# Kernel optimization log

Measured on AMD Instinct MI355X. Metric: run time of the kernel, lower is better.

The kernel has to match this reference:

```python
import jax, jax.numpy as jnp
import numpy as np

# Module config (from init_kwargs)
KH, KW = 3, 3          # kernel_size
SH, SW = 2, 2          # stride
PH, PW = 1, 1          # padding
EPS = 1e-8             # temperature clamp eps
DEN_EPS = 1e-12        # denominator stabilizer (hardcoded in kornia)
DN = ('NCHW', 'OIHW', 'NCHW')


def _window_grid_kernel(kh, kw):
    # window coordinates residual to window center, normalized to [-1, 1]
    ys, xs = jnp.meshgrid(jnp.arange(kh, dtype=jnp.float32),
                          jnp.arange(kw, dtype=jnp.float32), indexing='ij')
    gx = xs * (2.0 / (kw - 1)) - 1.0
    gy = ys * (2.0 / (kh - 1)) - 1.0
    return jnp.stack([gx, gy], axis=0)[:, None]  # (2,1,kh,kw), ch0=x, ch1=y


def _center_kernel(kh, kw):
    k = jnp.zeros((2, 2, kh, kw), jnp.float32)
    k = k.at[0, 0, kh // 2, kw // 2].set(1.0)
    k = k.at[1, 1, kh // 2, kw // 2].set(1.0)
    return k  # (2,2,kh,kw)


def _sum_pool(x):
    # pool_coef * avg_pool2d(count_include_pad=True) == windowed sum with zero pad
    return jax.lax.reduce_window(x, 0.0, jax.lax.add,
                                 (1, 1, KH, KW), (1, 1, SH, SW),
                                 [(0, 0), (0, 0), (PH, PH), (PW, PW)])


def setup_inputs() -> dict:
    key = jax.random.key(0)
    x = jax.random.normal(key, (8, 16, 512, 512), dtype=jnp.float32)
    temperature = jnp.ones((), dtype=jnp.float32)
    return {"x": x, "temperature": temperature}


def reference(x, temperature):
    b, c, h, w = x.shape
    xf = x.reshape(b * c, 1, h, w)

    x_exp = jnp.exp(xf / jnp.maximum(temperature, EPS))

    den = _sum_pool(x_exp) + DEN_EPS                     # (BC,1,Ho,Wo)
    resp_maxima = _sum_pool(x_exp * xf) / den            # softmax-pooled values

    # weighted sum of window-relative coordinates
    coords_num = jax.lax.conv_general_dilated(
        x_exp, _window_grid_kernel(KH, KW), (SH, SW),
        [(PH, PH), (PW, PW)], dimension_numbers=DN)      # (BC,2,Ho,Wo)

    # global grid (x, y) pixel coordinates, center-picked per window
    ys, xs = jnp.meshgrid(jnp.arange(h, dtype=jnp.float32),
                          jnp.arange(w, dtype=jnp.float32), indexing='ij')
    grid_global = jnp.stack([xs, ys], axis=0)[None]      # (1,2,h,w)
    grid_pooled = jax.lax.conv_general_dilated(
        grid_global, _center_kernel(KH, KW), (SH, SW),
        [(PH, PH), (PW, PW)], dimension_numbers=DN)      # (1,2,Ho,Wo)

    coords_max = coords_num / den + grid_pooled          # broadcast over BC

    # normalized_coordinates=True: map pixel coords to [-1, 1]
    cx = coords_max[:, 0] * (2.0 / (w - 1)) - 1.0
    cy = coords_max[:, 1] * (2.0 / (h - 1)) - 1.0
    coords_max = jnp.stack([cx, cy], axis=1)             # (BC,2,Ho,Wo)

    return coords_max, resp_maxima
```

## Files before the change

### kernel.cpp

```cpp
#include <hip/hip_runtime.h>


#define H  512
#define W  512
#define HO 256
#define WO 256
#define BC 128

typedef float v2f __attribute__((ext_vector_type(2)));

__global__ __launch_bounds__(256) void casm_kernel(
    const float* __restrict__ x, const float* __restrict__ temp,
    float* __restrict__ out)
{
    int nblk = gridDim.x;
    int bid  = blockIdx.x;
    int swz  = (bid & 7) * (nblk >> 3) + (bid >> 3);

    int idx = swz * 256 + (int)threadIdx.x;
    int t   = idx & 127;
    int ho  = (idx >> 7) & (HO - 1);
    int bc  = idx >> 15;

    float k = 1.44269504088896340736f / fmaxf(temp[0], 1e-8f);

    const float* __restrict__ xp = x + (size_t)bc * (H * W);
    int r0 = 2 * ho - 1;
    int cM = 4 * t;
    float mL = (t == 0) ? 0.0f : 1.0f;

    float den_a = 0.f, den_b = 0.f, cyn_a = 0.f, cyn_b = 0.f;
    float colL_a = 0.f, colR_a = 0.f, colL_b = 0.f, colR_b = 0.f;
    float num_a = 0.f, num_b = 0.f;

#pragma unroll
    for (int rr = 0; rr < 3; ++rr) {
        if (rr == 0 && r0 < 0) continue;
        const float* __restrict__ row = xp + (r0 + rr) * W;
        float4 v = *(const float4*)(row + cM);
        float vL = __shfl_up(v.w, 1);
        if ((t & 63) == 0 && t != 0) vL = row[cM - 1];
        float eL = mL * __builtin_amdgcn_exp2f(k * vL);
        float e0 = __builtin_amdgcn_exp2f(k * v.x);
        float e1 = __builtin_amdgcn_exp2f(k * v.y);
        float e2 = __builtin_amdgcn_exp2f(k * v.z);
        float e3 = __builtin_amdgcn_exp2f(k * v.w);
        float rs_a = eL + e0 + e1;
        float rs_b = e1 + e2 + e3;
        den_a += rs_a;  den_b += rs_b;
        if (rr == 0) { cyn_a -= rs_a; cyn_b -= rs_b; }
        if (rr == 2) { cyn_a += rs_a; cyn_b += rs_b; }
        colL_a += eL;  colR_a += e1;
        colL_b += e1;  colR_b += e3;
        num_a = fmaf(eL, vL, fmaf(e0, v.x, fmaf(e1, v.y, num_a)));
        num_b = fmaf(e1, v.y, fmaf(e2, v.z, fmaf(e3, v.w, num_b)));
    }

    float ia = __builtin_amdgcn_rcpf(den_a + 1e-12f);
    float ib = __builtin_amdgcn_rcpf(den_b + 1e-12f);
    const float scale = 2.0f / 511.0f;
    int wo0 = 2 * t;
    v2f vx = { ((colR_a - colL_a) * ia + (float)(2 * wo0    )) * scale - 1.0f,
               ((colR_b - colL_b) * ib + (float)(2 * wo0 + 2)) * scale - 1.0f };
    v2f vy = { (cyn_a * ia + (float)(2 * ho)) * scale - 1.0f,
               (cyn_b * ib + (float)(2 * ho)) * scale - 1.0f };
    v2f vr = { num_a * ia, num_b * ib };

    size_t pix   = (size_t)ho * WO + wo0;
    size_t cbase = (size_t)bc * (2 * HO * WO) + pix;
    __builtin_nontemporal_store(vx, (v2f*)(out + cbase));
    __builtin_nontemporal_store(vy, (v2f*)(out + cbase + HO * WO));
    __builtin_nontemporal_store(vr, (v2f*)(out + (size_t)BC * 2 * HO * WO
                                           + (size_t)bc * HO * WO + pix));
}

extern "C" void kernel_launch(void* const* d_in, const int* in_sizes, int n_in,
                              void* d_out, int out_size, void* d_ws, size_t ws_size,
                              hipStream_t stream) {
    const float* x    = (const float*)d_in[0];
    const float* temp = (const float*)d_in[1];
    float* out        = (float*)d_out;

    int total  = BC * HO * (WO / 2);
    int blocks = total / 256;
    casm_kernel<<<blocks, 256, 0, stream>>>(x, temp, out);
}
```

Baseline: 222.2 us.

## Compute two output rows per thread to share overlapping input row

Each thread now handles two vertically adjacent output rows, loading five input rows instead of three per output row, so the shared middle row's loads and exp computations are reused. The left-neighbour exp and product are shuffled from the adjacent lane instead of recomputing the exp, and nontemporal stores are replaced by plain float2 stores. This cuts redundant global reads and transcendental work by about a sixth and halves the grid, at the cost of more registers per thread and fewer threads in flight.

```diff
diff --git a/kernel.cpp b/kernel.cpp
--- a/kernel.cpp
+++ b/kernel.cpp
@@ -6,8 +6,6 @@
 #define HO 256
 #define WO 256
 #define BC 128
-
-typedef float v2f __attribute__((ext_vector_type(2)));
 
 __global__ __launch_bounds__(256) void casm_kernel(
     const float* __restrict__ x, const float* __restrict__ temp,
@@ -19,59 +17,101 @@
 
     int idx = swz * 256 + (int)threadIdx.x;
     int t   = idx & 127;
-    int ho  = (idx >> 7) & (HO - 1);
-    int bc  = idx >> 15;
+    int hp  = (idx >> 7) & 127;
+    int bc  = idx >> 14;
 
     float k = 1.44269504088896340736f / fmaxf(temp[0], 1e-8f);
 
     const float* __restrict__ xp = x + (size_t)bc * (H * W);
-    int r0 = 2 * ho - 1;
-    int cM = 4 * t;
-    float mL = (t == 0) ? 0.0f : 1.0f;
+    int  cM   = 4 * t;
+    float mL  = (t == 0) ? 0.0f : 1.0f;
+    bool bfix = ((t & 63) == 0) && (t != 0);
+    bool r0ok = (hp != 0);
 
-    float den_a = 0.f, den_b = 0.f, cyn_a = 0.f, cyn_b = 0.f;
-    float colL_a = 0.f, colR_a = 0.f, colL_b = 0.f, colR_b = 0.f;
-    float num_a = 0.f, num_b = 0.f;
+    const float* __restrict__ rb = xp + (size_t)(4 * hp) * W + cM;
+    float4 v0 = make_float4(0.f, 0.f, 0.f, 0.f);
+    if (r0ok) v0 = *(const float4*)(rb - W);
+    float4 v1 = *(const float4*)(rb);
+    float4 v2 = *(const float4*)(rb + W);
+    float4 v3 = *(const float4*)(rb + 2 * W);
+    float4 v4 = *(const float4*)(rb + 3 * W);
 
-#pragma unroll
-    for (int rr = 0; rr < 3; ++rr) {
-        if (rr == 0 && r0 < 0) continue;
-        const float* __restrict__ row = xp + (r0 + rr) * W;
-        float4 v = *(const float4*)(row + cM);
-        float vL = __shfl_up(v.w, 1);
-        if ((t & 63) == 0 && t != 0) vL = row[cM - 1];
-        float eL = mL * __builtin_amdgcn_exp2f(k * vL);
-        float e0 = __builtin_amdgcn_exp2f(k * v.x);
-        float e1 = __builtin_amdgcn_exp2f(k * v.y);
-        float e2 = __builtin_amdgcn_exp2f(k * v.z);
-        float e3 = __builtin_amdgcn_exp2f(k * v.w);
-        float rs_a = eL + e0 + e1;
-        float rs_b = e1 + e2 + e3;
-        den_a += rs_a;  den_b += rs_b;
-        if (rr == 0) { cyn_a -= rs_a; cyn_b -= rs_b; }
-        if (rr == 2) { cyn_a += rs_a; cyn_b += rs_b; }
-        colL_a += eL;  colR_a += e1;
-        colL_b += e1;  colR_b += e3;
-        num_a = fmaf(eL, vL, fmaf(e0, v.x, fmaf(e1, v.y, num_a)));
-        num_b = fmaf(e1, v.y, fmaf(e2, v.z, fmaf(e3, v.w, num_b)));
+#define EXPK(u) __builtin_amdgcn_exp2f(k * (u))
+#define ROW(v, rowp, rsA, rsB, dxA, dxB, nA, nB) {                       \
+        float e0 = EXPK((v).x), e1 = EXPK((v).y);                        \
+        float e2 = EXPK((v).z), e3 = EXPK((v).w);                        \
+        float p3 = e3 * (v).w;                                           \
+        float eL = __shfl_up(e3, 1);                                     \
+        float pL = __shfl_up(p3, 1);                                     \
+        if (bfix) { float vl = (rowp)[-1]; eL = EXPK(vl); pL = eL * vl; } \
+        eL *= mL; pL *= mL;                                              \
+        rsA = eL + e0 + e1;  rsB = e1 + e2 + e3;                         \
+        dxA = e1 - eL;       dxB = e3 - e1;                              \
+        nA  = pL + fmaf(e0, (v).x, e1 * (v).y);                          \
+        nB  = fmaf(e1, (v).y, fmaf(e2, (v).z, p3)); }
+
+    float rsA, rsB, dxA, dxB, nA, nB;
+
+    float d0A = 0, d0B = 0, cy0A = 0, cy0B = 0, x0A = 0, x0B = 0, m0A = 0, m0B = 0;
+    float d1A = 0, d1B = 0, cy1A = 0, cy1B = 0, x1A = 0, x1B = 0, m1A = 0, m1B = 0;
+
+    if (r0ok) {
+        ROW(v0, rb - W, rsA, rsB, dxA, dxB, nA, nB);
+        d0A += rsA; d0B += rsB; cy0A -= rsA; cy0B -= rsB;
+        x0A += dxA; x0B += dxB; m0A += nA;  m0B += nB;
     }
+    {
+        ROW(v1, rb, rsA, rsB, dxA, dxB, nA, nB);
+        d0A += rsA; d0B += rsB; x0A += dxA; x0B += dxB; m0A += nA; m0B += nB;
+    }
+    {
+        ROW(v2, rb + W, rsA, rsB, dxA, dxB, nA, nB);
+        d0A += rsA; d0B += rsB; cy0A += rsA; cy0B += rsB;
+        x0A += dxA; x0B += dxB; m0A += nA;  m0B += nB;
+        d1A += rsA; d1B += rsB; cy1A -= rsA; cy1B -= rsB;
+        x1A += dxA; x1B += dxB; m1A += nA;  m1B += nB;
+    }
+    {
+        ROW(v3, rb + 2 * W, rsA, rsB, dxA, dxB, nA, nB);
+        d1A += rsA; d1B += rsB; x1A += dxA; x1B += dxB; m1A += nA; m1B += nB;
+    }
+    {
+        ROW(v4, rb + 3 * W, rsA, rsB, dxA, dxB, nA, nB);
+        d1A += rsA; d1B += rsB; cy1A += rsA; cy1B += rsB;
+        x1A += dxA; x1B += dxB; m1A += nA;  m1B += nB;
+    }
+#undef ROW
+#undef EXPK
 
-    float ia = __builtin_amdgcn_rcpf(den_a + 1e-12f);
-    float ib = __builtin_amdgcn_rcpf(den_b + 1e-12f);
     const float scale = 2.0f / 511.0f;
     int wo0 = 2 * t;
-    v2f vx = { ((colR_a - colL_a) * ia + (float)(2 * wo0    )) * scale - 1.0f,
-               ((colR_b - colL_b) * ib + (float)(2 * wo0 + 2)) * scale - 1.0f };
-    v2f vy = { (cyn_a * ia + (float)(2 * ho)) * scale - 1.0f,
-               (cyn_b * ib + (float)(2 * ho)) * scale - 1.0f };
-    v2f vr = { num_a * ia, num_b * ib };
+    int ho0 = 2 * hp;
 
-    size_t pix   = (size_t)ho * WO + wo0;
-    size_t cbase = (size_t)bc * (2 * HO * WO) + pix;
-    __builtin_nontemporal_store(vx, (v2f*)(out + cbase));
-    __builtin_nontemporal_store(vy, (v2f*)(out + cbase + HO * WO));
-    __builtin_nontemporal_store(vr, (v2f*)(out + (size_t)BC * 2 * HO * WO
-                                           + (size_t)bc * HO * WO + pix));
+    float i0A = __builtin_amdgcn_rcpf(d0A + 1e-12f);
+    float i0B = __builtin_amdgcn_rcpf(d0B + 1e-12f);
+    float i1A = __builtin_amdgcn_rcpf(d1A + 1e-12f);
+    float i1B = __builtin_amdgcn_rcpf(d1B + 1e-12f);
+
+    size_t pix0  = (size_t)ho0 * WO + wo0;
+    size_t cbase = (size_t)bc * (2 * HO * WO);
+    size_t rbase = (size_t)BC * 2 * HO * WO + (size_t)bc * HO * WO;
+
+    *(float2*)(out + cbase + pix0) =
+        make_float2((x0A * i0A + (float)(2 * wo0)) * scale - 1.0f,
+                    (x0B * i0B + (float)(2 * wo0 + 2)) * scale - 1.0f);
+    *(float2*)(out + cbase + HO * WO + pix0) =
+        make_float2((cy0A * i0A + (float)(2 * ho0)) * scale - 1.0f,
+                    (cy0B * i0B + (float)(2 * ho0)) * scale - 1.0f);
+    *(float2*)(out + rbase + pix0) = make_float2(m0A * i0A, m0B * i0B);
+
+    size_t pix1 = pix0 + WO;
+    *(float2*)(out + cbase + pix1) =
+        make_float2((x1A * i1A + (float)(2 * wo0)) * scale - 1.0f,
+                    (x1B * i1B + (float)(2 * wo0 + 2)) * scale - 1.0f);
+    *(float2*)(out + cbase + HO * WO + pix1) =
+        make_float2((cy1A * i1A + (float)(2 * ho0 + 2)) * scale - 1.0f,
+                    (cy1B * i1B + (float)(2 * ho0 + 2)) * scale - 1.0f);
+    *(float2*)(out + rbase + pix1) = make_float2(m1A * i1A, m1B * i1B);
 }
 
 extern "C" void kernel_launch(void* const* d_in, const int* in_sizes, int n_in,
@@ -81,7 +121,7 @@
     const float* temp = (const float*)d_in[1];
     float* out        = (float*)d_out;
 
-    int total  = BC * HO * (WO / 2);
+    int total  = BC * (HO / 2) * (WO / 2);
     int blocks = total / 256;
     casm_kernel<<<blocks, 256, 0, stream>>>(x, temp, out);
 }
```

New measurement: 229.3 us. 1.03x slower.
